# Kernel tuning notes

Measured on AMD Instinct MI355X. Metric: run time of the kernel, lower is better.

The kernel has to match this reference:

```python
import jax, jax.numpy as jnp
import numpy as np

# --- static config (mirrors init_kwargs) ---
B, C, H, W = 32, 128, 16, 16
V = 8192                 # vocab_size
PNS = (1, 2, 4, 8, 16)   # v_patch_nums; last one == H == W
BETA = 0.25
RATIO = 0.5              # Phi resi_ratio
K_PHI = 4                # share_quant_resi: number of Phi conv blocks
_TICKS = np.linspace(1.0 / (3 * K_PHI), 1.0 - 1.0 / (3 * K_PHI), K_PHI)


def setup_inputs() -> dict:
    key = jax.random.key(0)
    k1, k2, k3 = jax.random.split(key, 3)
    f_BChw = jax.random.normal(k1, (B, C, H, W), jnp.float32)
    embedding = jax.random.normal(k2, (V, C), jnp.float32) * 0.5
    phi_w = jax.random.normal(k3, (K_PHI, C, C, 3, 3), jnp.float32) * 0.02
    phi_b = jnp.zeros((K_PHI, C), jnp.float32)
    return {"f_BChw": f_BChw, "embedding": embedding, "phi_w": phi_w, "phi_b": phi_b}


def _avg_pool(x, pn):
    # F.interpolate(mode='area') with divisible sizes == exact block mean
    b, c, h, w = x.shape
    return x.reshape(b, c, pn, h // pn, pn, w // pn).mean(axis=(3, 5))


def _phi(h, w, b):
    # Phi: x*(1-r) + conv3x3(x)*r
    y = jax.lax.conv_general_dilated(
        h, w, window_strides=(1, 1), padding='SAME',
        dimension_numbers=('NCHW', 'OIHW', 'NCHW'))
    y = y + b[None, :, None, None]
    return h * (1.0 - RATIO) + y * RATIO


def reference(f_BChw, embedding, phi_w, phi_b):
    f = f_BChw
    f_rest = jax.lax.stop_gradient(f)       # f_BChw.detach().clone()
    f_hat = jnp.zeros_like(f)
    SN = len(PNS)
    loss = jnp.float32(0.0)
    e_sq = jnp.sum(embedding ** 2, axis=1)  # [V]
    for si, pn in enumerate(PNS):
        rest = f_rest if si == SN - 1 else _avg_pool(f_rest, pn)
        rest_NC = rest.transpose(0, 2, 3, 1).reshape(-1, C)          # [B*pn*pn, C]
        # squared euclidean distance to codebook, argmin over V
        d = (jnp.sum(rest_NC ** 2, axis=1, keepdims=True) + e_sq
             - 2.0 * rest_NC @ embedding.T)                           # [N, V]
        idx = jnp.argmin(d, axis=1)                                   # [N]
        h = embedding[idx].reshape(B, pn, pn, C).transpose(0, 3, 1, 2)  # [B,C,pn,pn]
        if si != SN - 1:
            h = jax.image.resize(h, (B, C, H, W), method='cubic')     # bicubic upsample
        kphi = int(np.argmin(np.abs(_TICKS - si / (SN - 1))))
        h = _phi(h, phi_w[kphi], phi_b[kphi])
        f_hat = f_hat + h
        f_rest = f_rest - h
        loss = loss + (BETA * jnp.mean((jax.lax.stop_gradient(f_hat) - f) ** 2)
                       + jnp.mean((f_hat - jax.lax.stop_gradient(f)) ** 2))
    loss = loss / SN
    # straight-through: f_hat.data - f.detach() + f
    f_hat_out = jax.lax.stop_gradient(f_hat - f) + f
    return f_hat_out, loss
```

## Files before the change

kernel.cpp:

```cpp
#include <hip/hip_runtime.h>
#include <math.h>

#define CC   128
#define HH   16
#define WW   16
#define BB   32
#define VV   8192
#define NELEM (BB*CC*HH*WW)

typedef short short8 __attribute__((ext_vector_type(8)));
typedef float floatx4 __attribute__((ext_vector_type(4)));

#define CSTR 136

typedef __attribute__((address_space(1))) void as1_void;
typedef __attribute__((address_space(3))) void as3_void;

__device__ __forceinline__ void gl_lds16(const void* g, void* l) {
    __builtin_amdgcn_global_load_lds((as1_void*)g, (as3_void*)l, 16, 0, 0);
}

__device__ __forceinline__ uint32_t pack_hilo(float x) {
    uint32_t u = __float_as_uint(x);
    uint32_t hb = (u + 0x7fffu + ((u >> 16) & 1u)) & 0xffff0000u;
    float hf = __uint_as_float(hb);
    float lo = x - hf;
    uint32_t ul = __float_as_uint(lo);
    uint32_t lb = ((ul + 0x7fffu + ((ul >> 16) & 1u)) >> 16) & 0xffffu;
    return hb | lb;
}

__global__ void esq_pack(const float* __restrict__ emb, float* __restrict__ esq,
                         short* __restrict__ ephi, short* __restrict__ eplo,
                         float* __restrict__ lacc) {
    int t = blockIdx.x * 256 + threadIdx.x;
    int v = t >> 4, g = t & 15;
    const float* row = emb + (size_t)v * CC + g * 8;
    float4 a = *(const float4*)row;
    float4 b = *(const float4*)(row + 4);
    float s = a.x*a.x + a.y*a.y + a.z*a.z + a.w*a.w
            + b.x*b.x + b.y*b.y + b.z*b.z + b.w*b.w;
    s += __shfl_xor(s, 1, 64);
    s += __shfl_xor(s, 2, 64);
    s += __shfl_xor(s, 4, 64);
    s += __shfl_xor(s, 8, 64);
    if (g == 0) esq[v] = s;
    float vals[8] = {a.x, a.y, a.z, a.w, b.x, b.y, b.z, b.w};
    short hs[8], ls[8];
#pragma unroll
    for (int j = 0; j < 8; j++) {
        uint32_t u = pack_hilo(vals[j]);
        hs[j] = (short)(u >> 16);
        ls[j] = (short)(u & 0xffffu);
    }
    int vt = v >> 7, vr = v & 127;
    int vh = vr >> 6, tj = (vr >> 4) & 3, r15 = vr & 15;
    int kc = g >> 2, quad = g & 3;
    size_t off = (size_t)vt * 16384 + (size_t)((kc * 8 + vh * 4 + tj) * 64 + quad * 16 + r15) * 8;
    *(short8*)(ephi + off) = *(short8*)hs;
    *(short8*)(eplo + off) = *(short8*)ls;
    if (t == 0) lacc[0] = 0.f;
}

__global__ void prepack_w(const float* __restrict__ pw, short* __restrict__ Whi,
                          short* __restrict__ Wlo) {
    int id = blockIdx.x * 256 + threadIdx.x;
    int ci = id & 127, cout = (id >> 7) & 127, kp = id >> 14;
    const float* src = pw + ((size_t)(kp * CC + cout) * CC + ci) * 9;
#pragma unroll
    for (int kk = 0; kk < 9; kk++) {
        uint32_t u = pack_hilo(src[kk]);
        size_t o = ((size_t)(kp * 9 + kk) * CC + cout) * CC + ci;
        Whi[o] = (short)(u >> 16);
        Wlo[o] = (short)(u & 0xffffu);
    }
}

template <bool FIRSTP>
__global__ void pool_pack(const float* __restrict__ f, const float* __restrict__ fh,
                          short* __restrict__ rh, short* __restrict__ rl, int pn) {
    int id = blockIdx.x * 256 + threadIdx.x;
    int c = id % CC;
    int n = id / CC;
    int px = n % pn;
    int py = (n / pn) % pn;
    int b  = n / (pn * pn);
    int s  = HH / pn;
    size_t o = (((size_t)b * CC + c) * HH + py * s) * WW + px * s;
    float acc = 0.f;
    for (int dy = 0; dy < s; dy++)
        for (int dx = 0; dx < s; dx++)
            acc += FIRSTP ? f[o + dy * WW + dx] : (f[o + dy * WW + dx] - fh[o + dy * WW + dx]);
    uint32_t u = pack_hilo(acc * (1.f / (float)(s * s)));
    rh[id] = (short)(u >> 16);
    rl[id] = (short)(u & 0xffffu);
}

__global__ __launch_bounds__(512, 4)
void dist_mfma(const short* __restrict__ rphi, const short* __restrict__ rplo,
               const short* __restrict__ ephi, const short* __restrict__ eplo,
               const float* __restrict__ esq,
               float* __restrict__ pbD, int* __restrict__ pbI,
               int N, int vtPB) {
    __shared__ short Bs[2][2][8192];
    __shared__ float EsqL[1024];

    const int tid  = threadIdx.x;
    const int wave = tid >> 6, ln = tid & 63;
    const int quad = ln >> 4, l15 = ln & 15;
    const int qq = wave & 3, vh = wave >> 2;
    const int qb0 = blockIdx.x * 128;
    const int vslices = gridDim.y;
    const int vt0 = blockIdx.y * vtPB;
    const int nsteps = vtPB * 2;

#define STAGE_STEP(buf_, s_) do {                                                    \
        const int vt_ = vt0 + ((s_) >> 1);                                           \
        const int hf_ = (s_) & 1;                                                    \
        _Pragma("unroll")                                                            \
        for (int i_ = 0; i_ < 2; i_++) {                                             \
            const int ck_ = wave * 2 + i_;                                           \
            const int kc_ = ck_ >> 2, g_ = ck_ & 3;                                  \
            const size_t so_ = (size_t)vt_ * 32768 +                                 \
                               (size_t)(kc_ * 8 + hf_ * 4 + g_) * 1024;              \
            gl_lds16((const char*)ephi + so_ + ln * 16, (char*)&Bs[(buf_)][0][0] + ck_ * 1024); \
            gl_lds16((const char*)eplo + so_ + ln * 16, (char*)&Bs[(buf_)][1][0] + ck_ * 1024); \
        } } while (0)

    STAGE_STEP(0, 0);
    {
        int echunks = (vtPB * 512 + 1023) >> 10;
        if (wave < echunks)
            gl_lds16((const char*)(esq + vt0 * 128) + wave * 1024 + ln * 16,
                     (char*)EsqL + wave * 1024);
    }

    short8 av[2][4], aw[2][4];
#pragma unroll
    for (int ti = 0; ti < 2; ti++) {
        const size_t arow = (size_t)(qb0 + qq * 32 + ti * 16 + l15) * CC + quad * 8;
#pragma unroll
        for (int kc = 0; kc < 4; kc++) {
            av[ti][kc] = *(const short8*)(rphi + arow + kc * 32);
            aw[ti][kc] = *(const short8*)(rplo + arow + kc * 32);
        }
    }
    __builtin_amdgcn_sched_barrier(0);

    float bD[2][4];
    int   bI[2][4];
#pragma unroll
    for (int ti = 0; ti < 2; ti++)
#pragma unroll
        for (int r = 0; r < 4; r++) { bD[ti][r] = INFINITY; bI[ti][r] = 0; }

    int cur = 0;
    for (int s = 0; s < nsteps; s++) {
        if (s + 1 < nsteps) {
            STAGE_STEP(cur ^ 1, s + 1);
            asm volatile("s_waitcnt vmcnt(4)" ::: "memory");
        } else {
            asm volatile("s_waitcnt vmcnt(0)" ::: "memory");
        }
        __builtin_amdgcn_sched_barrier(0);
        __builtin_amdgcn_s_barrier();
        __builtin_amdgcn_sched_barrier(0);

        floatx4 acc[2][2];
        floatx4 z = {0.f, 0.f, 0.f, 0.f};
#pragma unroll
        for (int ti = 0; ti < 2; ti++)
#pragma unroll
            for (int tj = 0; tj < 2; tj++) acc[ti][tj] = z;

        const short* Bh = &Bs[cur][0][0];
        const short* Bl = &Bs[cur][1][0];
#pragma unroll
        for (int kc = 0; kc < 4; kc++) {
            short8 bh[2], bl[2];
#pragma unroll
            for (int tj = 0; tj < 2; tj++) {
                const int ck = kc * 4 + vh * 2 + tj;
                bh[tj] = *(const short8*)(Bh + ck * 512 + ln * 8);
                bl[tj] = *(const short8*)(Bl + ck * 512 + ln * 8);
            }
#pragma unroll
            for (int tj = 0; tj < 2; tj++)
#pragma unroll
                for (int ti = 0; ti < 2; ti++)
                    acc[ti][tj] = __builtin_amdgcn_mfma_f32_16x16x32_bf16(av[ti][kc], bh[tj], acc[ti][tj], 0, 0, 0);
#pragma unroll
            for (int tj = 0; tj < 2; tj++)
#pragma unroll
                for (int ti = 0; ti < 2; ti++)
                    acc[ti][tj] = __builtin_amdgcn_mfma_f32_16x16x32_bf16(aw[ti][kc], bh[tj], acc[ti][tj], 0, 0, 0);
#pragma unroll
            for (int tj = 0; tj < 2; tj++)
#pragma unroll
                for (int ti = 0; ti < 2; ti++)
                    acc[ti][tj] = __builtin_amdgcn_mfma_f32_16x16x32_bf16(av[ti][kc], bl[tj], acc[ti][tj], 0, 0, 0);
#pragma unroll
            for (int tj = 0; tj < 2; tj++)
#pragma unroll
                for (int ti = 0; ti < 2; ti++)
                    acc[ti][tj] = __builtin_amdgcn_mfma_f32_16x16x32_bf16(aw[ti][kc], bl[tj], acc[ti][tj], 0, 0, 0);
        }

        const int v0 = (vt0 + (s >> 1)) * 128 + (s & 1) * 64;
#pragma unroll
        for (int tj = 0; tj < 2; tj++) {
            int vg = v0 + vh * 32 + tj * 16 + l15;
            float ev = EsqL[s * 64 + vh * 32 + tj * 16 + l15];
#pragma unroll
            for (int ti = 0; ti < 2; ti++)
#pragma unroll
                for (int r = 0; r < 4; r++) {
                    float d = fmaf(-2.f, acc[ti][tj][r], ev);
                    if (d < bD[ti][r]) { bD[ti][r] = d; bI[ti][r] = vg; }
                }
        }

        __builtin_amdgcn_sched_barrier(0);
        __builtin_amdgcn_s_barrier();
        __builtin_amdgcn_sched_barrier(0);
        cur ^= 1;
    }
#undef STAGE_STEP

#pragma unroll
    for (int ti = 0; ti < 2; ti++)
#pragma unroll
        for (int r = 0; r < 4; r++) {
            float d = bD[ti][r];
            int   v = bI[ti][r];
#pragma unroll
            for (int m = 1; m <= 8; m <<= 1) {
                float od = __shfl_xor(d, m, 64);
                int   ov = __shfl_xor(v, m, 64);
                if (od < d || (od == d && ov < v)) { d = od; v = ov; }
            }
            if (l15 == 0) {
                int q = qb0 + qq * 32 + ti * 16 + quad * 4 + r;
                if (q < N) {
                    size_t o = (size_t)q * (vslices * 2) + blockIdx.y * 2 + vh;
                    pbD[o] = d;
                    pbI[o] = v;
                }
            }
        }
}

__device__ __forceinline__ float cubic_k(float x) {
    if (x <= 1.f) return (1.5f * x - 2.5f) * x * x + 1.f;
    if (x < 2.f)  return ((-0.5f * x + 2.5f) * x - 4.f) * x + 2.f;
    return 0.f;
}

template <int PN>
__global__ __launch_bounds__(256)
void upsample_pack(const float* __restrict__ emb,
                   const float* __restrict__ pbD, const int* __restrict__ pbI, int vsplit,
                   short* __restrict__ hhi, short* __restrict__ hlo,
                   float* __restrict__ hfp) {
    const int t = threadIdx.x;
    const int x = t & 15, y = t >> 4;
    const int b = blockIdx.x >> 4;
    const int c0 = (blockIdx.x & 15) * 8;

    float val[8];

    if constexpr (PN == 16) {
        int q = b * 256 + t;
        float bd = pbD[(size_t)q * vsplit];
        int   bi = pbI[(size_t)q * vsplit];
        for (int j = 1; j < vsplit; j++) {
            float d  = pbD[(size_t)q * vsplit + j];
            int   i2 = pbI[(size_t)q * vsplit + j];
            if (d < bd || (d == bd && i2 < bi)) { bd = d; bi = i2; }
        }
        float4 v0 = *(const float4*)(emb + (size_t)bi * CC + c0);
        float4 v1 = *(const float4*)(emb + (size_t)bi * CC + c0 + 4);
        val[0]=v0.x; val[1]=v0.y; val[2]=v0.z; val[3]=v0.w;
        val[4]=v1.x; val[5]=v1.y; val[6]=v1.z; val[7]=v1.w;
    } else {
        constexpr int NQ = PN * PN;
        constexpr int KK = 256 / NQ;
        __shared__ int idxL[NQ];
        __shared__ float S[NQ][8];
        __shared__ float prd[256];
        __shared__ int   pri[256];

        {
            const int qi = t & (NQ - 1);
            const int kk = t / NQ;
            float bd = INFINITY; int bi = 0;
            for (int j = kk; j < vsplit; j += KK) {
                float d  = pbD[(size_t)(b * NQ + qi) * vsplit + j];
                int   i2 = pbI[(size_t)(b * NQ + qi) * vsplit + j];
                if (d < bd || (d == bd && i2 < bi)) { bd = d; bi = i2; }
            }
            prd[t] = bd; pri[t] = bi;
        }
        __syncthreads();
        if (t < 64) {
            float d = prd[t]; int v = pri[t];
            for (int p = t + 64; p < 256; p += 64) {
                float d2 = prd[p]; int v2 = pri[p];
                if (d2 < d || (d2 == d && v2 < v)) { d = d2; v = v2; }
            }
#pragma unroll
            for (int m = NQ; m < 64; m <<= 1) {
                float d2 = __shfl_xor(d, m, 64);
                int   v2 = __shfl_xor(v, m, 64);
                if (d2 < d || (d2 == d && v2 < v)) { d = d2; v = v2; }
            }
            if (t < NQ) idxL[t] = v;
        }
        __syncthreads();
        if (t < NQ) {
            float4 v0 = *(const float4*)(emb + (size_t)idxL[t] * CC + c0);
            float4 v1 = *(const float4*)(emb + (size_t)idxL[t] * CC + c0 + 4);
            S[t][0]=v0.x; S[t][1]=v0.y; S[t][2]=v0.z; S[t][3]=v0.w;
            S[t][4]=v1.x; S[t][5]=v1.y; S[t][6]=v1.z; S[t][7]=v1.w;
        }
        __syncthreads();

        const float sc = (float)PN / 16.f;
        float sy = (y + 0.5f) * sc - 0.5f;
        float sx = (x + 0.5f) * sc - 0.5f;
        int iy0 = (int)floorf(sy) - 1;
        int ix0 = (int)floorf(sx) - 1;
        float wy[4], wx[4];
        float ssy = 0.f, ssx = 0.f;
#pragma unroll
        for (int k = 0; k < 4; k++) {
            int iy = iy0 + k, ix = ix0 + k;
            float a = (iy >= 0 && iy < PN) ? cubic_k(fabsf(sy - (float)iy)) : 0.f;
            float bb = (ix >= 0 && ix < PN) ? cubic_k(fabsf(sx - (float)ix)) : 0.f;
            wy[k] = a; ssy += a;
            wx[k] = bb; ssx += bb;
        }
        float ry = 1.f / ssy, rx = 1.f / ssx;
#pragma unroll
        for (int k = 0; k < 4; k++) { wy[k] *= ry; wx[k] *= rx; }

#pragma unroll
        for (int j = 0; j < 8; j++) val[j] = 0.f;
#pragma unroll
        for (int k4 = 0; k4 < 4; k4++) {
            int iy = iy0 + k4;
            if (iy < 0 || iy >= PN) continue;
#pragma unroll
            for (int j4 = 0; j4 < 4; j4++) {
                int ix = ix0 + j4;
                if (ix < 0 || ix >= PN) continue;
                float w = wy[k4] * wx[j4];
                const float* sp = S[iy * PN + ix];
#pragma unroll
                for (int j = 0; j < 8; j++) val[j] = fmaf(w, sp[j], val[j]);
            }
        }
    }

    short hs[8], ls[8];
#pragma unroll
    for (int j = 0; j < 8; j++) {
        uint32_t u = pack_hilo(val[j]);
        hs[j] = (short)(u >> 16);
        ls[j] = (short)(u & 0xffffu);
    }
    size_t ho = ((size_t)(b * 18 + y + 1) * 18 + (x + 1)) * CC + c0;
    *(short8*)(hhi + ho) = *(short8*)hs;
    *(short8*)(hlo + ho) = *(short8*)ls;
#pragma unroll
    for (int j = 0; j < 8; j++)
        hfp[((size_t)b * CC + c0 + j) * 256 + t] = val[j];
}

template <bool FIRST>
__global__ __launch_bounds__(256)
void conv_mfma(const short* __restrict__ Whi, const short* __restrict__ Wlo,
               const short* __restrict__ hhi, const short* __restrict__ hlo,
               const float* __restrict__ hfp, const float* __restrict__ pb,
               const float* __restrict__ f, float* __restrict__ f_hat,
               float* __restrict__ lacc, int kphi) {
    __shared__ short Bsh[64 * CSTR];
    __shared__ short Bsl[64 * CSTR];
    __shared__ float red[2][16][65];
    __shared__ float lred[2];

    const int t = threadIdx.x;
    const int wave = t >> 6, lane = t & 63;
    const int quad = lane >> 4, l15 = lane & 15;
    const int pxg = wave & 1, kh = wave >> 1;
    const int cH = blockIdx.x & 1;
    const int pc = blockIdx.x >> 1;
    const int b = pc >> 3;
    const int pxbase = (pc & 7) * 32;
    const int pa = pxbase + pxg * 16 + l15;
    const int ya = pa >> 4, xa = pa & 15;

    floatx4 acc[4];
    floatx4 z = {0.f, 0.f, 0.f, 0.f};
#pragma unroll
    for (int nt = 0; nt < 4; nt++) acc[nt] = z;

    for (int kk = 0; kk < 9; kk++) {
        __syncthreads();
        {
            const short* gh = Whi + ((size_t)(kphi * 9 + kk) * CC + cH * 64) * CC;
            const short* gl = Wlo + ((size_t)(kphi * 9 + kk) * CC + cH * 64) * CC;
#pragma unroll
            for (int i = 0; i < 4; i++) {
                int chunk = i * 256 + t;
                int row = chunk >> 4, col = (chunk & 15) * 8;
                *(short8*)&Bsh[row * CSTR + col] = *(const short8*)(gh + row * CC + col);
                *(short8*)&Bsl[row * CSTR + col] = *(const short8*)(gl + row * CC + col);
            }
        }
        __syncthreads();

        const int ky = kk / 3, kx = kk % 3;
        const size_t aoff = ((size_t)(b * 18 + ya + ky) * 18 + (xa + kx)) * CC + quad * 8;
#pragma unroll
        for (int i2 = 0; i2 < 2; i2++) {
            const int cic = kh * 2 + i2;
            short8 ah = *(const short8*)(hhi + aoff + cic * 32);
            short8 al = *(const short8*)(hlo + aoff + cic * 32);
#pragma unroll
            for (int nt = 0; nt < 4; nt++) {
                short8 bh = *(const short8*)&Bsh[(nt * 16 + l15) * CSTR + cic * 32 + quad * 8];
                short8 bl = *(const short8*)&Bsl[(nt * 16 + l15) * CSTR + cic * 32 + quad * 8];
                acc[nt] = __builtin_amdgcn_mfma_f32_16x16x32_bf16(ah, bh, acc[nt], 0, 0, 0);
                acc[nt] = __builtin_amdgcn_mfma_f32_16x16x32_bf16(al, bh, acc[nt], 0, 0, 0);
                acc[nt] = __builtin_amdgcn_mfma_f32_16x16x32_bf16(ah, bl, acc[nt], 0, 0, 0);
            }
        }
    }

    __syncthreads();
    if (kh == 1) {
#pragma unroll
        for (int nt = 0; nt < 4; nt++)
#pragma unroll
            for (int r = 0; r < 4; r++)
                red[pxg][quad * 4 + r][nt * 16 + l15] = acc[nt][r];
    }
    __syncthreads();

    if (kh == 0) {
        const int pe = pxbase + pxg * 16 + quad * 4;
        float lsum = 0.f;
#pragma unroll
        for (int nt = 0; nt < 4; nt++) {
            int cout = cH * 64 + nt * 16 + l15;
            float bias = pb[kphi * CC + cout];
            size_t gi = ((size_t)b * CC + cout) * 256 + pe;
            float4 h4  = *(const float4*)(hfp + gi);
            float4 f4  = *(const float4*)(f + gi);
            float4 fh4 = FIRST ? make_float4(0.f, 0.f, 0.f, 0.f) : *(const float4*)(f_hat + gi);
            float c0 = acc[nt][0] + red[pxg][quad * 4 + 0][nt * 16 + l15] + bias;
            float c1 = acc[nt][1] + red[pxg][quad * 4 + 1][nt * 16 + l15] + bias;
            float c2 = acc[nt][2] + red[pxg][quad * 4 + 2][nt * 16 + l15] + bias;
            float c3 = acc[nt][3] + red[pxg][quad * 4 + 3][nt * 16 + l15] + bias;
            float o0 = fh4.x + 0.5f * h4.x + 0.5f * c0;
            float o1 = fh4.y + 0.5f * h4.y + 0.5f * c1;
            float o2 = fh4.z + 0.5f * h4.z + 0.5f * c2;
            float o3 = fh4.w + 0.5f * h4.w + 0.5f * c3;
            *(float4*)(f_hat + gi) = make_float4(o0, o1, o2, o3);
            float d0 = o0 - f4.x, d1 = o1 - f4.y, d2 = o2 - f4.z, d3 = o3 - f4.w;
            lsum += d0*d0 + d1*d1 + d2*d2 + d3*d3;
        }
#pragma unroll
        for (int off = 32; off; off >>= 1) lsum += __shfl_down(lsum, off, 64);
        if (lane == 0) lred[pxg] = lsum;
    }
    __syncthreads();
    if (t == 0) atomicAdd(lacc, lred[0] + lred[1]);
}

__global__ void finalize_kernel(const float* __restrict__ lacc, float* __restrict__ out_loss) {
    *out_loss = lacc[0] * (0.25f / (float)NELEM);
}

extern "C" void kernel_launch(void* const* d_in, const int* in_sizes, int n_in,
                              void* d_out, int out_size, void* d_ws, size_t ws_size,
                              hipStream_t stream) {
    const float* f   = (const float*)d_in[0];
    const float* emb = (const float*)d_in[1];
    const float* pw  = (const float*)d_in[2];
    const float* pb  = (const float*)d_in[3];
    float* out = (float*)d_out;

    uint32_t* w32 = (uint32_t*)d_ws;
    short* rphi = (short*)(w32);
    short* rplo = (short*)(w32 + 524288);
    short* ephi = (short*)(w32 + 1048576);
    short* eplo = (short*)(w32 + 1572864);
    short* Whi  = (short*)(w32 + 2097152);
    short* Wlo  = (short*)(w32 + 2392064);
    short* hhi  = (short*)(w32 + 2686976);
    short* hlo  = (short*)(w32 + 3350528);
    float* hfp  = (float*)(w32 + 4014080);
    float* esq  = (float*)(w32 + 5062656);
    float* pbD  = (float*)(w32 + 5070848);
    int*   pbI  = (int*)  (w32 + 5332992);
    float* lacc = (float*)(w32 + 5595136);

    hipMemsetAsync(hhi, 0, (size_t)2 * 1327104 * sizeof(short), stream);

    esq_pack<<<512, 256, 0, stream>>>(emb, esq, ephi, eplo, lacc);
    prepack_w<<<256, 256, 0, stream>>>(pw, Whi, Wlo);

    double start = 1.0 / 12.0;
    double stop  = 1.0 - 1.0 / 12.0;
    double step  = (stop - start) / 3.0;
    double ticks[4] = {start, 1.0 * step + start, 2.0 * step + start, stop};

    const int pns[5]    = {1, 2, 4, 8, 16};
    const int qb5[5]    = {1, 1, 4, 16, 64};
    const int vs5[5]    = {64, 64, 64, 32, 8};
    const int vtPB5[5]  = {1, 1, 1, 2, 8};

    for (int si = 0; si < 5; si++) {
        int pn = pns[si];
        int N  = BB * pn * pn;
        double tt = (double)si / 4.0;
        int kphi = 0;
        double bd = fabs(ticks[0] - tt);
        for (int i = 1; i < 4; i++) {
            double d = fabs(ticks[i] - tt);
            if (d < bd) { bd = d; kphi = i; }
        }

        if (si == 0) pool_pack<true><<<(N * CC) / 256, 256, 0, stream>>>(f, out, rphi, rplo, pn);
        else         pool_pack<false><<<(N * CC) / 256, 256, 0, stream>>>(f, out, rphi, rplo, pn);

        dim3 dgrid(qb5[si], vs5[si]);
        dist_mfma<<<dgrid, 512, 0, stream>>>(rphi, rplo, ephi, eplo, esq, pbD, pbI, N, vtPB5[si]);

        int vsplit = vs5[si] * 2;
        switch (pn) {
            case 1:  upsample_pack<1><<<512, 256, 0, stream>>>(emb, pbD, pbI, vsplit, hhi, hlo, hfp); break;
            case 2:  upsample_pack<2><<<512, 256, 0, stream>>>(emb, pbD, pbI, vsplit, hhi, hlo, hfp); break;
            case 4:  upsample_pack<4><<<512, 256, 0, stream>>>(emb, pbD, pbI, vsplit, hhi, hlo, hfp); break;
            case 8:  upsample_pack<8><<<512, 256, 0, stream>>>(emb, pbD, pbI, vsplit, hhi, hlo, hfp); break;
            default: upsample_pack<16><<<512, 256, 0, stream>>>(emb, pbD, pbI, vsplit, hhi, hlo, hfp); break;
        }

        if (si == 0) conv_mfma<true><<<512, 256, 0, stream>>>(Whi, Wlo, hhi, hlo, hfp, pb, f, out, lacc, kphi);
        else         conv_mfma<false><<<512, 256, 0, stream>>>(Whi, Wlo, hhi, hlo, hfp, pb, f, out, lacc, kphi);
    }

    finalize_kernel<<<1, 1, 0, stream>>>(lacc, out + NELEM);
}
```

Before: 437.4 us.

## Halve dist_mfma query tile to 64 rows and vocab step to 32 for occupancy

Shrinks the distance-argmin MFMA kernel's block tile from 128 queries by 64 codes per step to 64 queries by 32 codes per step. LDS per block and register arrays are halved, and launch bounds are raised to allow 8 blocks per CU. The query grid is doubled to match. The aim is more resident waves and better latency hiding. The cost is twice as many barrier-separated steps and less reuse of each staged codebook tile across queries.

Measured after the change: 431.5 us. No clear change (-1.3%).

```diff
diff --git a/kernel.cpp b/kernel.cpp
--- a/kernel.cpp
+++ b/kernel.cpp
@@ -96,36 +96,33 @@
     rl[id] = (short)(u & 0xffffu);
 }
 
-__global__ __launch_bounds__(512, 4)
+__global__ __launch_bounds__(512, 8)
 void dist_mfma(const short* __restrict__ rphi, const short* __restrict__ rplo,
                const short* __restrict__ ephi, const short* __restrict__ eplo,
                const float* __restrict__ esq,
                float* __restrict__ pbD, int* __restrict__ pbI,
                int N, int vtPB) {
-    __shared__ short Bs[2][2][8192];
+    __shared__ short Bs[2][2][4096];
     __shared__ float EsqL[1024];
 
     const int tid  = threadIdx.x;
     const int wave = tid >> 6, ln = tid & 63;
     const int quad = ln >> 4, l15 = ln & 15;
     const int qq = wave & 3, vh = wave >> 2;
-    const int qb0 = blockIdx.x * 128;
+    const int qb0 = blockIdx.x * 64;
     const int vslices = gridDim.y;
     const int vt0 = blockIdx.y * vtPB;
-    const int nsteps = vtPB * 2;
+    const int nsteps = vtPB * 4;
 
 #define STAGE_STEP(buf_, s_) do {                                                    \
-        const int vt_ = vt0 + ((s_) >> 1);                                           \
-        const int hf_ = (s_) & 1;                                                    \
-        _Pragma("unroll")                                                            \
-        for (int i_ = 0; i_ < 2; i_++) {                                             \
-            const int ck_ = wave * 2 + i_;                                           \
-            const int kc_ = ck_ >> 2, g_ = ck_ & 3;                                  \
-            const size_t so_ = (size_t)vt_ * 32768 +                                 \
-                               (size_t)(kc_ * 8 + hf_ * 4 + g_) * 1024;              \
-            gl_lds16((const char*)ephi + so_ + ln * 16, (char*)&Bs[(buf_)][0][0] + ck_ * 1024); \
-            gl_lds16((const char*)eplo + so_ + ln * 16, (char*)&Bs[(buf_)][1][0] + ck_ * 1024); \
-        } } while (0)
+        const int vt_  = vt0 + ((s_) >> 2);                                          \
+        const int q32_ = (s_) & 3;                                                   \
+        const int kc_  = wave >> 1, t_ = wave & 1;                                   \
+        const size_t so_ = (size_t)vt_ * 32768 +                                     \
+                           (size_t)(kc_ * 8 + q32_ * 2 + t_) * 1024;                 \
+        gl_lds16((const char*)ephi + so_ + ln * 16, (char*)&Bs[(buf_)][0][0] + wave * 1024); \
+        gl_lds16((const char*)eplo + so_ + ln * 16, (char*)&Bs[(buf_)][1][0] + wave * 1024); \
+    } while (0)
 
     STAGE_STEP(0, 0);
     {
@@ -135,30 +132,27 @@
                      (char*)EsqL + wave * 1024);
     }
 
-    short8 av[2][4], aw[2][4];
-#pragma unroll
-    for (int ti = 0; ti < 2; ti++) {
-        const size_t arow = (size_t)(qb0 + qq * 32 + ti * 16 + l15) * CC + quad * 8;
+    short8 av[4], aw[4];
+    {
+        const size_t arow = (size_t)(qb0 + qq * 16 + l15) * CC + quad * 8;
 #pragma unroll
         for (int kc = 0; kc < 4; kc++) {
-            av[ti][kc] = *(const short8*)(rphi + arow + kc * 32);
-            aw[ti][kc] = *(const short8*)(rplo + arow + kc * 32);
+            av[kc] = *(const short8*)(rphi + arow + kc * 32);
+            aw[kc] = *(const short8*)(rplo + arow + kc * 32);
         }
     }
     __builtin_amdgcn_sched_barrier(0);
 
-    float bD[2][4];
-    int   bI[2][4];
-#pragma unroll
-    for (int ti = 0; ti < 2; ti++)
-#pragma unroll
-        for (int r = 0; r < 4; r++) { bD[ti][r] = INFINITY; bI[ti][r] = 0; }
+    float bD[4];
+    int   bI[4];
+#pragma unroll
+    for (int r = 0; r < 4; r++) { bD[r] = INFINITY; bI[r] = 0; }
 
     int cur = 0;
     for (int s = 0; s < nsteps; s++) {
         if (s + 1 < nsteps) {
             STAGE_STEP(cur ^ 1, s + 1);
-            asm volatile("s_waitcnt vmcnt(4)" ::: "memory");
+            asm volatile("s_waitcnt vmcnt(2)" ::: "memory");
         } else {
             asm volatile("s_waitcnt vmcnt(0)" ::: "memory");
         }
@@ -166,58 +160,29 @@
         __builtin_amdgcn_s_barrier();
         __builtin_amdgcn_sched_barrier(0);
 
-        floatx4 acc[2][2];
-        floatx4 z = {0.f, 0.f, 0.f, 0.f};
-#pragma unroll
-        for (int ti = 0; ti < 2; ti++)
-#pragma unroll
-            for (int tj = 0; tj < 2; tj++) acc[ti][tj] = z;
+        floatx4 acc = {0.f, 0.f, 0.f, 0.f};
 
         const short* Bh = &Bs[cur][0][0];
         const short* Bl = &Bs[cur][1][0];
 #pragma unroll
         for (int kc = 0; kc < 4; kc++) {
-            short8 bh[2], bl[2];
-#pragma unroll
-            for (int tj = 0; tj < 2; tj++) {
-                const int ck = kc * 4 + vh * 2 + tj;
-                bh[tj] = *(const short8*)(Bh + ck * 512 + ln * 8);
-                bl[tj] = *(const short8*)(Bl + ck * 512 + ln * 8);
-            }
-#pragma unroll
-            for (int tj = 0; tj < 2; tj++)
-#pragma unroll
-                for (int ti = 0; ti < 2; ti++)
-                    acc[ti][tj] = __builtin_amdgcn_mfma_f32_16x16x32_bf16(av[ti][kc], bh[tj], acc[ti][tj], 0, 0, 0);
-#pragma unroll
-            for (int tj = 0; tj < 2; tj++)
-#pragma unroll
-                for (int ti = 0; ti < 2; ti++)
-                    acc[ti][tj] = __builtin_amdgcn_mfma_f32_16x16x32_bf16(aw[ti][kc], bh[tj], acc[ti][tj], 0, 0, 0);
-#pragma unroll
-            for (int tj = 0; tj < 2; tj++)
-#pragma unroll
-                for (int ti = 0; ti < 2; ti++)
-                    acc[ti][tj] = __builtin_amdgcn_mfma_f32_16x16x32_bf16(av[ti][kc], bl[tj], acc[ti][tj], 0, 0, 0);
-#pragma unroll
-            for (int tj = 0; tj < 2; tj++)
-#pragma unroll
-                for (int ti = 0; ti < 2; ti++)
-                    acc[ti][tj] = __builtin_amdgcn_mfma_f32_16x16x32_bf16(aw[ti][kc], bl[tj], acc[ti][tj], 0, 0, 0);
-        }
-
-        const int v0 = (vt0 + (s >> 1)) * 128 + (s & 1) * 64;
-#pragma unroll
-        for (int tj = 0; tj < 2; tj++) {
-            int vg = v0 + vh * 32 + tj * 16 + l15;
-            float ev = EsqL[s * 64 + vh * 32 + tj * 16 + l15];
-#pragma unroll
-            for (int ti = 0; ti < 2; ti++)
-#pragma unroll
-                for (int r = 0; r < 4; r++) {
-                    float d = fmaf(-2.f, acc[ti][tj][r], ev);
-                    if (d < bD[ti][r]) { bD[ti][r] = d; bI[ti][r] = vg; }
-                }
+            const int ck = kc * 2 + vh;
+            short8 bh = *(const short8*)(Bh + ck * 512 + ln * 8);
+            short8 bl = *(const short8*)(Bl + ck * 512 + ln * 8);
+            acc = __builtin_amdgcn_mfma_f32_16x16x32_bf16(av[kc], bh, acc, 0, 0, 0);
+            acc = __builtin_amdgcn_mfma_f32_16x16x32_bf16(aw[kc], bh, acc, 0, 0, 0);
+            acc = __builtin_amdgcn_mfma_f32_16x16x32_bf16(av[kc], bl, acc, 0, 0, 0);
+            acc = __builtin_amdgcn_mfma_f32_16x16x32_bf16(aw[kc], bl, acc, 0, 0, 0);
+        }
+
+        const int vg = vt0 * 128 + s * 32 + vh * 16 + l15;
+        {
+            float ev = EsqL[s * 32 + vh * 16 + l15];
+#pragma unroll
+            for (int r = 0; r < 4; r++) {
+                float d = fmaf(-2.f, acc[r], ev);
+                if (d < bD[r]) { bD[r] = d; bI[r] = vg; }
+            }
         }
 
         __builtin_amdgcn_sched_barrier(0);
@@ -228,26 +193,24 @@
 #undef STAGE_STEP
 
 #pragma unroll
-    for (int ti = 0; ti < 2; ti++)
-#pragma unroll
-        for (int r = 0; r < 4; r++) {
-            float d = bD[ti][r];
-            int   v = bI[ti][r];
-#pragma unroll
-            for (int m = 1; m <= 8; m <<= 1) {
-                float od = __shfl_xor(d, m, 64);
-                int   ov = __shfl_xor(v, m, 64);
-                if (od < d || (od == d && ov < v)) { d = od; v = ov; }
-            }
-            if (l15 == 0) {
-                int q = qb0 + qq * 32 + ti * 16 + quad * 4 + r;
-                if (q < N) {
-                    size_t o = (size_t)q * (vslices * 2) + blockIdx.y * 2 + vh;
-                    pbD[o] = d;
-                    pbI[o] = v;
-                }
-            }
-        }
+    for (int r = 0; r < 4; r++) {
+        float d = bD[r];
+        int   v = bI[r];
+#pragma unroll
+        for (int m = 1; m <= 8; m <<= 1) {
+            float od = __shfl_xor(d, m, 64);
+            int   ov = __shfl_xor(v, m, 64);
+            if (od < d || (od == d && ov < v)) { d = od; v = ov; }
+        }
+        if (l15 == 0) {
+            int q = qb0 + qq * 16 + quad * 4 + r;
+            if (q < N) {
+                size_t o = (size_t)q * (vslices * 2) + blockIdx.y * 2 + vh;
+                pbD[o] = d;
+                pbI[o] = v;
+            }
+        }
+    }
 }
 
 __device__ __forceinline__ float cubic_k(float x) {
@@ -518,7 +481,7 @@
     double ticks[4] = {start, 1.0 * step + start, 2.0 * step + start, stop};
 
     const int pns[5]    = {1, 2, 4, 8, 16};
-    const int qb5[5]    = {1, 1, 4, 16, 64};
+    const int qb5[5]    = {1, 2, 8, 32, 128};
     const int vs5[5]    = {64, 64, 64, 32, 8};
     const int vtPB5[5]  = {1, 1, 1, 2, 8};
 
```
